# Performance work log

Measured on AMD Instinct MI355X. Metric: run time of the kernel, lower is better.

The kernel has to match this reference:

```python
import jax, jax.numpy as jnp
import numpy as np

B, N, D, H = 4, 4096, 1024, 16
DH = D // H          # per-head dim = 64
M = 256              # number of random features
KEPS = 1e-3          # performer kernel epsilon
LNEPS = 1e-5


def setup_inputs() -> dict:
    key = jax.random.key(0)
    ks = jax.random.split(key, 16)
    s = 0.02
    return {
        "src": jax.random.normal(ks[0], (B, N, D), jnp.float32),
        "Wq": s * jax.random.normal(ks[1], (D, D), jnp.float32),
        "Wk": s * jax.random.normal(ks[2], (D, D), jnp.float32),
        "Wv": s * jax.random.normal(ks[3], (D, D), jnp.float32),
        "Wout": s * jax.random.normal(ks[4], (D, D), jnp.float32),
        "b_out": jnp.zeros((D,), jnp.float32),
        "proj": jax.random.normal(ks[5], (M, DH), jnp.float32),
        "g1": jnp.ones((D,), jnp.float32),
        "beta1": jnp.zeros((D,), jnp.float32),
        "W1": s * jax.random.normal(ks[6], (2048, D), jnp.float32),
        "b1": jnp.zeros((2048,), jnp.float32),
        "W2": s * jax.random.normal(ks[7], (D, 2048), jnp.float32),
        "b2": jnp.zeros((D,), jnp.float32),
        "g2": jnp.ones((D,), jnp.float32),
        "beta2": jnp.zeros((D,), jnp.float32),
    }


def _layernorm(x, g, b):
    mu = x.mean(-1, keepdims=True)
    var = ((x - mu) ** 2).mean(-1, keepdims=True)
    return (x - mu) * jax.lax.rsqrt(var + LNEPS) * g + b


def _softmax_kernel(x, proj, is_query):
    # FAVOR+ positive softmax kernel feature map (performer_pytorch)
    dn = DH ** -0.25           # data normalizer d^{-1/4}
    ratio = M ** -0.5
    data_dash = jnp.einsum('bhnd,md->bhnm', x * dn, proj)
    diag = (x ** 2).sum(-1) * 0.5 * dn * dn            # [b,h,n]
    if is_query:
        stab = data_dash.max(-1, keepdims=True)
    else:
        stab = data_dash.max()
    return ratio * (jnp.exp(data_dash - diag[..., None] - stab) + KEPS)


def reference(src, Wq, Wk, Wv, Wout, b_out, proj, g1, beta1, W1, b1, W2, b2, g2, beta2):
    # ---- Performer self-attention (FAVOR+, non-causal) ----
    def split_heads(x):
        return x.reshape(B, N, H, DH).transpose(0, 2, 1, 3)  # [b,h,n,dh]

    q = split_heads(src @ Wq.T)
    k = split_heads(src @ Wk.T)
    v = split_heads(src @ Wv.T)

    qp = _softmax_kernel(q, proj, is_query=True)   # [b,h,n,m]
    kp = _softmax_kernel(k, proj, is_query=False)  # [b,h,n,m]

    k_sum = kp.sum(-2)                                        # [b,h,m]
    d_inv = 1.0 / jnp.einsum('bhnm,bhm->bhn', qp, k_sum)      # [b,h,n]
    context = jnp.einsum('bhnm,bhnd->bhmd', kp, v)            # [b,h,m,dh]
    attn = jnp.einsum('bhnm,bhmd->bhnd', qp, context) * d_inv[..., None]

    attn = attn.transpose(0, 2, 1, 3).reshape(B, N, D)
    src2 = attn @ Wout.T + b_out

    # ---- residual + norm + FFN (dropout = identity at eval) ----
    x = _layernorm(src + src2, g1, beta1)
    ff = (jax.nn.gelu(x @ W1.T + b1, approximate=False)) @ W2.T + b2
    return _layernorm(x + ff, g2, beta2)
```

## Files before the change

kernel.cpp:

```cpp
#include <hip/hip_runtime.h>

#define DEVI __device__ __forceinline__

using u16 = unsigned short;
using u32 = unsigned int;
using u64 = unsigned long long;

typedef __bf16 bf16x8 __attribute__((ext_vector_type(8)));
typedef float  f32x4  __attribute__((ext_vector_type(4)));

constexpr int BB = 4, NN = 4096, DD = 1024, HH = 16, DH = 64, MF = 256;
constexpr int RT = BB * NN;
constexpr int QKVS = 3072;
constexpr float DN    = 0.35355339059327373f;
constexpr float RATIO = 0.0625f;
constexpr float DIAGC = 0.0625f;
constexpr float KEPSC = 1e-3f;

DEVI u16 f2bf(float f) {
  u32 u = __float_as_uint(f);
  u32 r = u + 0x7fffu + ((u >> 16) & 1u);
  return (u16)(r >> 16);
}
DEVI float bf2f(u16 u) { return __uint_as_float(((u32)u) << 16); }

typedef void __attribute__((address_space(1)))* gas1;
typedef void __attribute__((address_space(3)))* las3;
DEVI void gload_lds16(const void* g, void* l) {
  __builtin_amdgcn_global_load_lds((gas1)(u64)g, (las3)(u32)(u64)l, 16, 0, 0);
}

DEVI bf16x8 ldswz(const u16* base, int row, int kbyte) {
  int p = (row << 7) + kbyte;
  p ^= (row & 7) << 4;
  return *(const bf16x8*)((const char*)base + p);
}

__global__ void cast_kernel(const float* __restrict__ in, u16* __restrict__ out, int n4) {
  int i = blockIdx.x * 256 + threadIdx.x;
  int stride = gridDim.x * 256;
  for (; i < n4; i += stride) {
    float4 v = ((const float4*)in)[i];
    ushort4 o; o.x = f2bf(v.x); o.y = f2bf(v.y); o.z = f2bf(v.z); o.w = f2bf(v.w);
    ((ushort4*)out)[i] = o;
  }
}

__global__ void cast_proj_kernel(const float* __restrict__ in, u16* __restrict__ out) {
  int i = blockIdx.x * 256 + threadIdx.x;
  float4 v = ((const float4*)in)[i];
  ushort4 o; o.x = f2bf(v.x * DN); o.y = f2bf(v.y * DN); o.z = f2bf(v.z * DN); o.w = f2bf(v.w * DN);
  ((ushort4*)out)[i] = o;
}

template <int EPI>
__global__ __launch_bounds__(256, 2) void gemm_bt(
    const u16* __restrict__ A, const u16* __restrict__ Bm,
    u16* __restrict__ Cb, const float* __restrict__ bias,
    int Ncols, int K)
{
  __shared__ __align__(16) u16 sA[128 * 64];
  __shared__ __align__(16) u16 sB[128 * 64];
  const int tid = threadIdx.x, lane = tid & 63;
  const int wv = tid >> 6, wr = wv >> 1, wc = wv & 1;
  const int bm = blockIdx.y, bn = blockIdx.x;

  f32x4 acc[4][4] = {};

  int rowS[4], colS[4], ldsb[4];
#pragma unroll
  for (int it = 0; it < 4; ++it) {
    int p = (it * 256 + tid) * 16;
    ldsb[it] = (it * 256 + (tid & ~63)) * 16;
    int sp = p ^ (((p >> 7) & 7) << 4);
    rowS[it] = sp >> 7;
    colS[it] = (sp >> 1) & 63;
  }
  const size_t baseA = (size_t)bm * 128, baseB = (size_t)bn * 128;

  for (int kt = 0; kt < K; kt += 64) {
#pragma unroll
    for (int it = 0; it < 4; ++it)
      gload_lds16(A + (baseA + rowS[it]) * K + kt + colS[it], (char*)sA + ldsb[it]);
#pragma unroll
    for (int it = 0; it < 4; ++it)
      gload_lds16(Bm + (baseB + rowS[it]) * K + kt + colS[it], (char*)sB + ldsb[it]);
    __syncthreads();
#pragma unroll
    for (int kk = 0; kk < 2; ++kk) {
      const int kbyte = kk * 64 + ((lane >> 4) << 4);
      bf16x8 a[4], b[4];
#pragma unroll
      for (int i = 0; i < 4; ++i) a[i] = ldswz(sA, wr * 64 + i * 16 + (lane & 15), kbyte);
#pragma unroll
      for (int i = 0; i < 4; ++i) b[i] = ldswz(sB, wc * 64 + i * 16 + (lane & 15), kbyte);
#pragma unroll
      for (int i = 0; i < 4; ++i)
#pragma unroll
        for (int j = 0; j < 4; ++j)
          acc[i][j] = __builtin_amdgcn_mfma_f32_16x16x32_bf16(a[i], b[j], acc[i][j], 0, 0, 0);
    }
    __syncthreads();
  }

#pragma unroll
  for (int i = 0; i < 4; ++i) {
    const int gr0 = bm * 128 + wr * 64 + i * 16 + ((lane >> 4) << 2);
#pragma unroll
    for (int j = 0; j < 4; ++j) {
      const int gc = bn * 128 + wc * 64 + j * 16 + (lane & 15);
#pragma unroll
      for (int r = 0; r < 4; ++r) {
        const size_t o = (size_t)(gr0 + r) * Ncols + gc;
        const float v = acc[i][j][r];
        if constexpr (EPI == 0) {
          Cb[o] = f2bf(v);
        } else if constexpr (EPI == 2) {
          float t = v + bias[gc];
          Cb[o] = f2bf(0.5f * t * (1.0f + erff(t * 0.70710678118654752f)));
        } else {
          Cb[o] = f2bf(v + bias[gc]);
        }
      }
    }
  }
}

__global__ __launch_bounds__(256) void kmax_kernel(
    const u16* __restrict__ qkvb, const u16* __restrict__ projb, float* __restrict__ pmax)
{
  __shared__ __align__(16) u16 sX[64 * 72];
  __shared__ float sred[4];
  const int tid = threadIdx.x, lane = tid & 63, wv = tid >> 6;
  const int bh = blockIdx.x, b = bh >> 4, h = bh & 15;
  const int n0 = blockIdx.y * 64;

  for (int i = tid; i < 512; i += 256) {
    int r = i >> 3, c8 = (i & 7) << 3;
    uint4 v = *(const uint4*)(qkvb + ((size_t)(b * NN + n0 + r)) * QKVS + 1024 + h * DH + c8);
    *(uint4*)&sX[r * 72 + c8] = v;
  }
  __syncthreads();

  f32x4 dacc[16] = {};
#pragma unroll
  for (int kk = 0; kk < 2; ++kk) {
    const int ko = kk * 32 + ((lane >> 4) << 3);
    bf16x8 a = *(const bf16x8*)&sX[(wv * 16 + (lane & 15)) * 72 + ko];
#pragma unroll
    for (int f = 0; f < 16; ++f) {
      bf16x8 bb = *(const bf16x8*)(projb + (f * 16 + (lane & 15)) * 64 + ko);
      dacc[f] = __builtin_amdgcn_mfma_f32_16x16x32_bf16(a, bb, dacc[f], 0, 0, 0);
    }
  }
  float mx = -1e30f;
#pragma unroll
  for (int f = 0; f < 16; ++f)
#pragma unroll
    for (int r = 0; r < 4; ++r) mx = fmaxf(mx, dacc[f][r]);
#pragma unroll
  for (int m = 1; m < 64; m <<= 1) mx = fmaxf(mx, __shfl_xor(mx, m));
  if (lane == 0) sred[wv] = mx;
  __syncthreads();
  if (tid == 0)
    pmax[blockIdx.y * gridDim.x + blockIdx.x] =
        fmaxf(fmaxf(sred[0], sred[1]), fmaxf(sred[2], sred[3]));
}

__global__ __launch_bounds__(256) void reduce_max_kernel(
    const float* __restrict__ pmax, float* __restrict__ stab)
{
  const int tid = threadIdx.x;
  float mx = -1e30f;
#pragma unroll
  for (int i = 0; i < 16; ++i) mx = fmaxf(mx, pmax[i * 256 + tid]);
#pragma unroll
  for (int m = 1; m < 64; m <<= 1) mx = fmaxf(mx, __shfl_xor(mx, m));
  __shared__ float sred[4];
  if ((tid & 63) == 0) sred[tid >> 6] = mx;
  __syncthreads();
  if (tid == 0)
    stab[0] = fmaxf(fmaxf(sred[0], sred[1]), fmaxf(sred[2], sred[3]));
}

__global__ __launch_bounds__(256, 1) void kctx_kernel(
    const u16* __restrict__ qkvb, const u16* __restrict__ projb,
    const float* __restrict__ stab_p,
    float* __restrict__ ctxP, float* __restrict__ ksumP2)
{
  __shared__ __align__(16) u16 sX[64 * 72];
  __shared__ __align__(16) u16 sVT[64 * 72];
  __shared__ __align__(16) u16 sKpT[256 * 72];
  __shared__ float sDiag[64];
  const int tid = threadIdx.x, lane = tid & 63, wv = tid >> 6;
  const int bh = blockIdx.x, b = bh >> 4, h = bh & 15;
  const int sl = blockIdx.y;
  const float stab = stab_p[0];

  f32x4 cacc[16] = {};
  float ksacc[16] = {};
  const int row_base = wv * 16 + ((lane >> 4) << 2);

  for (int t = 0; t < 8; ++t) {
    const int n0 = sl * 512 + t * 64;
    if (t) __syncthreads();
    for (int i = tid; i < 512; i += 256) {
      int r = i >> 3, c8 = (i & 7) << 3;
      size_t g = ((size_t)(b * NN + n0 + r)) * QKVS + h * DH + c8;
      uint4 xv = *(const uint4*)(qkvb + g + 1024);
      *(uint4*)&sX[r * 72 + c8] = xv;
      uint4 vv = *(const uint4*)(qkvb + g + 2048);
      const u16* pv = (const u16*)&vv;
#pragma unroll
      for (int j = 0; j < 8; ++j) sVT[(c8 + j) * 72 + r] = pv[j];
    }
    __syncthreads();
    {
      int r = tid >> 2, qq = tid & 3;
      float s = 0;
#pragma unroll
      for (int j = 0; j < 16; ++j) { float x = bf2f(sX[r * 72 + qq * 16 + j]); s += x * x; }
      s += __shfl_xor(s, 1); s += __shfl_xor(s, 2);
      if (qq == 0) sDiag[r] = DIAGC * s;
    }
    f32x4 dacc[16] = {};
#pragma unroll
    for (int kk = 0; kk < 2; ++kk) {
      const int ko = kk * 32 + ((lane >> 4) << 3);
      bf16x8 a = *(const bf16x8*)&sX[(wv * 16 + (lane & 15)) * 72 + ko];
#pragma unroll
      for (int f = 0; f < 16; ++f) {
        bf16x8 bb = *(const bf16x8*)(projb + (f * 16 + (lane & 15)) * 64 + ko);
        dacc[f] = __builtin_amdgcn_mfma_f32_16x16x32_bf16(a, bb, dacc[f], 0, 0, 0);
      }
    }
    __syncthreads();
#pragma unroll
    for (int f = 0; f < 16; ++f) {
      float kvv[4]; float cs = 0;
#pragma unroll
      for (int r = 0; r < 4; ++r) {
        float val = RATIO * (__expf(dacc[f][r] - sDiag[row_base + r] - stab) + KEPSC);
        kvv[r] = val; cs += val;
      }
      cs += __shfl_xor(cs, 16); cs += __shfl_xor(cs, 32);
      ksacc[f] += cs;
      ushort4 pk; pk.x = f2bf(kvv[0]); pk.y = f2bf(kvv[1]); pk.z = f2bf(kvv[2]); pk.w = f2bf(kvv[3]);
      *(ushort4*)&sKpT[(f * 16 + (lane & 15)) * 72 + row_base] = pk;
    }
    __syncthreads();
#pragma unroll
    for (int kk = 0; kk < 2; ++kk) {
      const int ko = kk * 32 + ((lane >> 4) << 3);
      bf16x8 a = *(const bf16x8*)&sVT[(wv * 16 + (lane & 15)) * 72 + ko];
#pragma unroll
      for (int f = 0; f < 16; ++f) {
        bf16x8 bb = *(const bf16x8*)&sKpT[(f * 16 + (lane & 15)) * 72 + ko];
        cacc[f] = __builtin_amdgcn_mfma_f32_16x16x32_bf16(a, bb, cacc[f], 0, 0, 0);
      }
    }
  }
  float* cp = ctxP + (size_t)(sl * 64 + bh) * 16384;
#pragma unroll
  for (int f = 0; f < 16; ++f) {
    const int m = f * 16 + (lane & 15);
#pragma unroll
    for (int r = 0; r < 4; ++r)
      cp[(row_base + r) * 256 + m] = cacc[f][r];
  }
  if (lane < 16) {
    float* kp = ksumP2 + (size_t)((sl * 64 + bh) * 4 + wv) * 256;
#pragma unroll
    for (int f = 0; f < 16; ++f) kp[f * 16 + lane] = ksacc[f];
  }
}

__global__ __launch_bounds__(256) void ctxfin_kernel(
    const float* __restrict__ ctxP, const float* __restrict__ ksumP2,
    u16* __restrict__ ctxb, float* __restrict__ ksum)
{
  const int bid = blockIdx.x, tid = threadIdx.x;
  if (bid < 1024) {
    const int idx = bid * 256 + tid;
    const int bh = idx >> 12, pos = idx & 4095;
    float4 s = {0, 0, 0, 0};
#pragma unroll
    for (int sl = 0; sl < 8; ++sl) {
      float4 v = *(const float4*)(ctxP + (size_t)(sl * 64 + bh) * 16384 + pos * 4);
      s.x += v.x; s.y += v.y; s.z += v.z; s.w += v.w;
    }
    ushort4 o; o.x = f2bf(s.x); o.y = f2bf(s.y); o.z = f2bf(s.z); o.w = f2bf(s.w);
    *(ushort4*)(ctxb + (size_t)bh * 16384 + pos * 4) = o;
  } else {
    const int idx = (bid - 1024) * 256 + tid;
    const int bh = idx >> 8, m = idx & 255;
    float s = 0;
#pragma unroll
    for (int sl = 0; sl < 8; ++sl)
#pragma unroll
      for (int w = 0; w < 4; ++w)
        s += ksumP2[(size_t)((sl * 64 + bh) * 4 + w) * 256 + m];
    ksum[idx] = s;
  }
}

__global__ __launch_bounds__(256, 2) void qattn_kernel(
    const u16* __restrict__ qkvb, const u16* __restrict__ projb,
    const u16* __restrict__ ctxb, const float* __restrict__ ksum,
    u16* __restrict__ attnb)
{
  __shared__ __align__(16) u16 sCtx[64 * 256];
  __shared__ __align__(16) u16 sX[64 * 72];
  __shared__ __align__(16) u16 sQp[64 * 264];
  __shared__ float sKsum[256];
  __shared__ float sDiag[64];
  __shared__ float sDinv[64];
  const int tid = threadIdx.x, lane = tid & 63, wv = tid >> 6;
  const int bh = blockIdx.x, b = bh >> 4, h = bh & 15;

  {
    const char* cbase = (const char*)(ctxb + (size_t)bh * 16384);
#pragma unroll
    for (int it = 0; it < 8; ++it) {
      int p = (it * 256 + tid) * 16;
      int ldsb = (it * 256 + (tid & ~63)) * 16;
      int q = p ^ (((p >> 9) & 7) << 4);
      gload_lds16(cbase + q, (char*)sCtx + ldsb);
    }
  }
  sKsum[tid] = ksum[bh * 256 + tid];

  const int row_base = wv * 16 + ((lane >> 4) << 2);
  const int wr = wv >> 1, wc = wv & 1;

  for (int rt = 0; rt < 2; ++rt) {
    const int n0 = (blockIdx.y * 2 + rt) * 64;
    for (int i = tid; i < 512; i += 256) {
      int r = i >> 3, c8 = (i & 7) << 3;
      uint4 v = *(const uint4*)(qkvb + ((size_t)(b * NN + n0 + r)) * QKVS + h * DH + c8);
      *(uint4*)&sX[r * 72 + c8] = v;
    }
    __syncthreads();
    {
      int r = tid >> 2, qq = tid & 3;
      float s = 0;
#pragma unroll
      for (int j = 0; j < 16; ++j) { float x = bf2f(sX[r * 72 + qq * 16 + j]); s += x * x; }
      s += __shfl_xor(s, 1); s += __shfl_xor(s, 2);
      if (qq == 0) sDiag[r] = DIAGC * s;
    }
    f32x4 dacc[16] = {};
#pragma unroll
    for (int kk = 0; kk < 2; ++kk) {
      const int ko = kk * 32 + ((lane >> 4) << 3);
      bf16x8 a = *(const bf16x8*)&sX[(wv * 16 + (lane & 15)) * 72 + ko];
#pragma unroll
      for (int f = 0; f < 16; ++f) {
        bf16x8 bb = *(const bf16x8*)(projb + (f * 16 + (lane & 15)) * 64 + ko);
        dacc[f] = __builtin_amdgcn_mfma_f32_16x16x32_bf16(a, bb, dacc[f], 0, 0, 0);
      }
    }
    __syncthreads();
#pragma unroll
    for (int r = 0; r < 4; ++r) {
      const int row = row_base + r;
      float mx = dacc[0][r];
#pragma unroll
      for (int f = 1; f < 16; ++f) mx = fmaxf(mx, dacc[f][r]);
      mx = fmaxf(mx, __shfl_xor(mx, 1));
      mx = fmaxf(mx, __shfl_xor(mx, 2));
      mx = fmaxf(mx, __shfl_xor(mx, 4));
      mx = fmaxf(mx, __shfl_xor(mx, 8));
      const float dg = sDiag[row];
      float ds = 0;
#pragma unroll
      for (int f = 0; f < 16; ++f) {
        float qv = RATIO * (__expf(dacc[f][r] - dg - mx) + KEPSC);
        dacc[f][r] = qv;
        ds += qv * sKsum[f * 16 + (lane & 15)];
      }
      ds += __shfl_xor(ds, 1); ds += __shfl_xor(ds, 2);
      ds += __shfl_xor(ds, 4); ds += __shfl_xor(ds, 8);
      if ((lane & 15) == 0) sDinv[row] = 1.0f / ds;
    }
#pragma unroll
    for (int f = 0; f < 16; ++f)
#pragma unroll
      for (int r = 0; r < 4; ++r)
        sQp[(row_base + r) * 264 + f * 16 + (lane & 15)] = f2bf(dacc[f][r]);
    __syncthreads();

    f32x4 acc2[2][2] = {};
#pragma unroll
    for (int kk = 0; kk < 8; ++kk) {
      const int koe = kk * 32 + ((lane >> 4) << 3);
      const int kob = koe * 2;
      bf16x8 a0 = *(const bf16x8*)&sQp[(wr * 32 + (lane & 15)) * 264 + koe];
      bf16x8 a1 = *(const bf16x8*)&sQp[(wr * 32 + 16 + (lane & 15)) * 264 + koe];
      const int j0 = wc * 32 + (lane & 15), j1 = j0 + 16;
      bf16x8 b0 = *(const bf16x8*)((const char*)sCtx + (((j0 << 9) + kob) ^ ((j0 & 7) << 4)));
      bf16x8 b1 = *(const bf16x8*)((const char*)sCtx + (((j1 << 9) + kob) ^ ((j1 & 7) << 4)));
      acc2[0][0] = __builtin_amdgcn_mfma_f32_16x16x32_bf16(a0, b0, acc2[0][0], 0, 0, 0);
      acc2[0][1] = __builtin_amdgcn_mfma_f32_16x16x32_bf16(a0, b1, acc2[0][1], 0, 0, 0);
      acc2[1][0] = __builtin_amdgcn_mfma_f32_16x16x32_bf16(a1, b0, acc2[1][0], 0, 0, 0);
      acc2[1][1] = __builtin_amdgcn_mfma_f32_16x16x32_bf16(a1, b1, acc2[1][1], 0, 0, 0);
    }
#pragma unroll
    for (int mi = 0; mi < 2; ++mi)
#pragma unroll
      for (int ni = 0; ni < 2; ++ni)
#pragma unroll
        for (int r = 0; r < 4; ++r) {
          const int row = wr * 32 + mi * 16 + ((lane >> 4) << 2) + r;
          const int col = wc * 32 + ni * 16 + (lane & 15);
          float v = acc2[mi][ni][r] * sDinv[row];
          attnb[((size_t)(b * NN + n0 + row)) * DD + h * DH + col] = f2bf(v);
        }
    __syncthreads();
  }
}

__global__ __launch_bounds__(256) void ln1_kernel(
    const float* __restrict__ src, const u16* __restrict__ wout,
    const float* __restrict__ g, const float* __restrict__ be, u16* __restrict__ xb)
{
  const int row = blockIdx.x, tid = threadIdx.x;
  const float4 sv = ((const float4*)(src + (size_t)row * DD))[tid];
  const ushort4 wv = ((const ushort4*)(wout + (size_t)row * DD))[tid];
  float x0 = sv.x + bf2f(wv.x);
  float x1 = sv.y + bf2f(wv.y);
  float x2 = sv.z + bf2f(wv.z);
  float x3 = sv.w + bf2f(wv.w);
  float s = x0 + x1 + x2 + x3;
  float ss = x0 * x0 + x1 * x1 + x2 * x2 + x3 * x3;
#pragma unroll
  for (int m = 1; m < 64; m <<= 1) { s += __shfl_xor(s, m); ss += __shfl_xor(ss, m); }
  __shared__ float red[8];
  if ((tid & 63) == 0) { red[tid >> 6] = s; red[4 + (tid >> 6)] = ss; }
  __syncthreads();
  s = red[0] + red[1] + red[2] + red[3];
  ss = red[4] + red[5] + red[6] + red[7];
  const float mu = s * (1.0f / DD);
  const float rs = rsqrtf(ss * (1.0f / DD) - mu * mu + 1e-5f);
  const float4 gv = ((const float4*)g)[tid];
  const float4 bv = ((const float4*)be)[tid];
  ushort4 o;
  o.x = f2bf((x0 - mu) * rs * gv.x + bv.x);
  o.y = f2bf((x1 - mu) * rs * gv.y + bv.y);
  o.z = f2bf((x2 - mu) * rs * gv.z + bv.z);
  o.w = f2bf((x3 - mu) * rs * gv.w + bv.w);
  ((ushort4*)(xb + (size_t)row * DD))[tid] = o;
}

__global__ __launch_bounds__(256) void ln2_kernel(
    const u16* __restrict__ xb, const u16* __restrict__ ff,
    const float* __restrict__ g, const float* __restrict__ be, float* __restrict__ out)
{
  const int row = blockIdx.x, tid = threadIdx.x;
  const ushort4 xv = ((const ushort4*)(xb + (size_t)row * DD))[tid];
  const ushort4 fv = ((const ushort4*)(ff + (size_t)row * DD))[tid];
  float x0 = bf2f(xv.x) + bf2f(fv.x);
  float x1 = bf2f(xv.y) + bf2f(fv.y);
  float x2 = bf2f(xv.z) + bf2f(fv.z);
  float x3 = bf2f(xv.w) + bf2f(fv.w);
  float s = x0 + x1 + x2 + x3;
  float ss = x0 * x0 + x1 * x1 + x2 * x2 + x3 * x3;
#pragma unroll
  for (int m = 1; m < 64; m <<= 1) { s += __shfl_xor(s, m); ss += __shfl_xor(ss, m); }
  __shared__ float red[8];
  if ((tid & 63) == 0) { red[tid >> 6] = s; red[4 + (tid >> 6)] = ss; }
  __syncthreads();
  s = red[0] + red[1] + red[2] + red[3];
  ss = red[4] + red[5] + red[6] + red[7];
  const float mu = s * (1.0f / DD);
  const float rs = rsqrtf(ss * (1.0f / DD) - mu * mu + 1e-5f);
  const float4 gv = ((const float4*)g)[tid];
  const float4 bv = ((const float4*)be)[tid];
  float4 o;
  o.x = (x0 - mu) * rs * gv.x + bv.x;
  o.y = (x1 - mu) * rs * gv.y + bv.y;
  o.z = (x2 - mu) * rs * gv.z + bv.z;
  o.w = (x3 - mu) * rs * gv.w + bv.w;
  ((float4*)(out + (size_t)row * DD))[tid] = o;
}

extern "C" void kernel_launch(void* const* d_in, const int* in_sizes, int n_in,
                              void* d_out, int out_size, void* d_ws, size_t ws_size,
                              hipStream_t stream) {
  (void)in_sizes; (void)n_in; (void)out_size; (void)ws_size;
  const float* src   = (const float*)d_in[0];
  const float* Wq    = (const float*)d_in[1];
  const float* Wk    = (const float*)d_in[2];
  const float* Wv    = (const float*)d_in[3];
  const float* Wout  = (const float*)d_in[4];
  const float* b_out = (const float*)d_in[5];
  const float* proj  = (const float*)d_in[6];
  const float* g1    = (const float*)d_in[7];
  const float* be1   = (const float*)d_in[8];
  const float* W1    = (const float*)d_in[9];
  const float* b1    = (const float*)d_in[10];
  const float* W2    = (const float*)d_in[11];
  const float* b2    = (const float*)d_in[12];
  const float* g2    = (const float*)d_in[13];
  const float* be2   = (const float*)d_in[14];

  char* ws = (char*)d_ws;
  constexpr size_t OFF_SRCB = 0;
  constexpr size_t OFF_QKV  = 33554432;
  constexpr size_t OFF_WOUTB= 100663296;
  constexpr size_t OFF_WQ   = 134217728;
  constexpr size_t OFF_WO   = 140509184;
  constexpr size_t OFF_W1   = 142606336;
  constexpr size_t OFF_W2   = 146800640;
  constexpr size_t OFF_PROJ = 150994944;
  constexpr size_t OFF_CTXB = 151027712;
  constexpr size_t OFF_KSUM = 153124864;
  constexpr size_t OFF_KSP2 = 153190400;
  constexpr size_t OFF_PMAX = 155287552;
  constexpr size_t OFF_STAB = 155303936;

  u16* srcb  = (u16*)(ws + OFF_SRCB);
  u16* qkvb  = (u16*)(ws + OFF_QKV);
  u16* wqkvb = (u16*)(ws + OFF_WQ);
  u16* wob   = (u16*)(ws + OFF_WO);
  u16* w1b   = (u16*)(ws + OFF_W1);
  u16* w2b   = (u16*)(ws + OFF_W2);
  u16* projb = (u16*)(ws + OFF_PROJ);
  u16* ctxb  = (u16*)(ws + OFF_CTXB);
  float* ksum  = (float*)(ws + OFF_KSUM);
  float* ksumP2= (float*)(ws + OFF_KSP2);
  float* pmax  = (float*)(ws + OFF_PMAX);
  float* stab  = (float*)(ws + OFF_STAB);
  float* ctxP  = (float*)(ws + OFF_SRCB);
  u16* attnb = (u16*)(ws + OFF_SRCB);
  u16* woutb = (u16*)(ws + OFF_WOUTB);
  u16* xb    = (u16*)(ws + OFF_QKV + 33554432);
  u16* h1    = (u16*)(ws + OFF_SRCB);
  u16* ff    = (u16*)(ws + OFF_WOUTB);

  cast_kernel<<<4096, 256, 0, stream>>>(src, srcb, RT * DD / 4);
  cast_kernel<<<1024, 256, 0, stream>>>(Wq, wqkvb, DD * DD / 4);
  cast_kernel<<<1024, 256, 0, stream>>>(Wk, wqkvb + DD * DD, DD * DD / 4);
  cast_kernel<<<1024, 256, 0, stream>>>(Wv, wqkvb + 2 * DD * DD, DD * DD / 4);
  cast_kernel<<<1024, 256, 0, stream>>>(Wout, wob, DD * DD / 4);
  cast_kernel<<<2048, 256, 0, stream>>>(W1, w1b, 2048 * DD / 4);
  cast_kernel<<<2048, 256, 0, stream>>>(W2, w2b, 2048 * DD / 4);
  cast_proj_kernel<<<16, 256, 0, stream>>>(proj, projb);

  gemm_bt<0><<<dim3(QKVS / 128, RT / 128), 256, 0, stream>>>(srcb, wqkvb, qkvb, nullptr, QKVS, DD);

  kmax_kernel<<<dim3(64, 64), 256, 0, stream>>>(qkvb, projb, pmax);
  reduce_max_kernel<<<1, 256, 0, stream>>>(pmax, stab);
  kctx_kernel<<<dim3(64, 8), 256, 0, stream>>>(qkvb, projb, stab, ctxP, ksumP2);
  ctxfin_kernel<<<1088, 256, 0, stream>>>(ctxP, ksumP2, ctxb, ksum);
  qattn_kernel<<<dim3(64, 32), 256, 0, stream>>>(qkvb, projb, ctxb, ksum, attnb);

  gemm_bt<3><<<dim3(DD / 128, RT / 128), 256, 0, stream>>>(attnb, wob, woutb, b_out, DD, DD);
  ln1_kernel<<<RT, 256, 0, stream>>>(src, woutb, g1, be1, xb);

  gemm_bt<2><<<dim3(2048 / 128, RT / 128), 256, 0, stream>>>(xb, w1b, h1, b1, 2048, DD);
  gemm_bt<3><<<dim3(DD / 128, RT / 128), 256, 0, stream>>>(h1, w2b, ff, b2, DD, 2048);
  ln2_kernel<<<RT, 256, 0, stream>>>(xb, ff, g2, be2, (float*)d_out);
}
```

Before: 787.0 us.

## Enlarge GEMM tiles, fuse weight casts, atomically reduce context, reuse QKV buffer

The GEMM now uses 512-thread blocks with 256x128 tiles, an lda parameter, and a workgroup swizzle so neighbouring blocks share L2. The six weight casts and the proj cast are merged into one grid-stride kernel. kctx now accumulates the context and k_sum straight into zeroed buffers with atomicAdd, which shrinks ctxfin to a plain bf16 cast. qattn writes its output in place into the Q columns of the QKV buffer, and the output projection reads it with stride 3072. The aim is to cut launch count, partial-sum traffic and A-operand reloads, at the cost of atomic contention, higher register and LDS pressure per block, and nondeterministic float summation.

```diff
diff --git a/kernel.cpp b/kernel.cpp
--- a/kernel.cpp
+++ b/kernel.cpp
@@ -46,44 +46,68 @@
   }
 }
 
-__global__ void cast_proj_kernel(const float* __restrict__ in, u16* __restrict__ out) {
+__global__ void cast_weights_kernel(
+    const float* __restrict__ Wq, const float* __restrict__ Wk,
+    const float* __restrict__ Wv, const float* __restrict__ Wout,
+    const float* __restrict__ W1, const float* __restrict__ W2,
+    const float* __restrict__ proj,
+    u16* __restrict__ wqkvb, u16* __restrict__ wob,
+    u16* __restrict__ w1b, u16* __restrict__ w2b, u16* __restrict__ projb)
+{
+  constexpr int TOT = 2101248;
   int i = blockIdx.x * 256 + threadIdx.x;
-  float4 v = ((const float4*)in)[i];
-  ushort4 o; o.x = f2bf(v.x * DN); o.y = f2bf(v.y * DN); o.z = f2bf(v.z * DN); o.w = f2bf(v.w * DN);
-  ((ushort4*)out)[i] = o;
+  const int stride = gridDim.x * 256;
+  for (; i < TOT; i += stride) {
+    const float* s; u16* d; int loc; float sc = 1.0f;
+    if (i < 1048576) {
+      int seg = i >> 18; loc = i & 262143;
+      s = (seg == 0) ? Wq : (seg == 1) ? Wk : (seg == 2) ? Wv : Wout;
+      d = (seg < 3) ? (wqkvb + seg * 1048576) : wob;
+    } else if (i < 1572864) { loc = i - 1048576; s = W1; d = w1b; }
+    else if (i < 2097152)   { loc = i - 1572864; s = W2; d = w2b; }
+    else                    { loc = i - 2097152; s = proj; d = projb; sc = DN; }
+    float4 v = ((const float4*)s)[loc];
+    ushort4 o; o.x = f2bf(v.x * sc); o.y = f2bf(v.y * sc); o.z = f2bf(v.z * sc); o.w = f2bf(v.w * sc);
+    ((ushort4*)d)[loc] = o;
+  }
 }
 
 template <int EPI>
-__global__ __launch_bounds__(256, 2) void gemm_bt(
-    const u16* __restrict__ A, const u16* __restrict__ Bm,
+__global__ __launch_bounds__(512, 4) void gemm_bt(
+    const u16* __restrict__ A, int lda, const u16* __restrict__ Bm,
     u16* __restrict__ Cb, const float* __restrict__ bias,
     int Ncols, int K)
 {
-  __shared__ __align__(16) u16 sA[128 * 64];
+  __shared__ __align__(16) u16 sA[256 * 64];
   __shared__ __align__(16) u16 sB[128 * 64];
   const int tid = threadIdx.x, lane = tid & 63;
   const int wv = tid >> 6, wr = wv >> 1, wc = wv & 1;
-  const int bm = blockIdx.y, bn = blockIdx.x;
+
+  const int gx = gridDim.x;
+  const int wg = blockIdx.y * gx + blockIdx.x;
+  const int cpx = (gx * gridDim.y) >> 3;
+  const int swz = (wg & 7) * cpx + (wg >> 3);
+  const int bn = swz % gx, bm = swz / gx;
 
   f32x4 acc[4][4] = {};
 
   int rowS[4], colS[4], ldsb[4];
 #pragma unroll
   for (int it = 0; it < 4; ++it) {
-    int p = (it * 256 + tid) * 16;
-    ldsb[it] = (it * 256 + (tid & ~63)) * 16;
+    int p = (it * 512 + tid) * 16;
+    ldsb[it] = (it * 512 + (tid & ~63)) * 16;
     int sp = p ^ (((p >> 7) & 7) << 4);
     rowS[it] = sp >> 7;
     colS[it] = (sp >> 1) & 63;
   }
-  const size_t baseA = (size_t)bm * 128, baseB = (size_t)bn * 128;
+  const size_t baseA = (size_t)bm * 256, baseB = (size_t)bn * 128;
 
   for (int kt = 0; kt < K; kt += 64) {
 #pragma unroll
     for (int it = 0; it < 4; ++it)
-      gload_lds16(A + (baseA + rowS[it]) * K + kt + colS[it], (char*)sA + ldsb[it]);
-#pragma unroll
-    for (int it = 0; it < 4; ++it)
+      gload_lds16(A + (baseA + rowS[it]) * lda + kt + colS[it], (char*)sA + ldsb[it]);
+#pragma unroll
+    for (int it = 0; it < 2; ++it)
       gload_lds16(Bm + (baseB + rowS[it]) * K + kt + colS[it], (char*)sB + ldsb[it]);
     __syncthreads();
 #pragma unroll
@@ -105,7 +129,7 @@
 
 #pragma unroll
   for (int i = 0; i < 4; ++i) {
-    const int gr0 = bm * 128 + wr * 64 + i * 16 + ((lane >> 4) << 2);
+    const int gr0 = bm * 256 + wr * 64 + i * 16 + ((lane >> 4) << 2);
 #pragma unroll
     for (int j = 0; j < 4; ++j) {
       const int gc = bn * 128 + wc * 64 + j * 16 + (lane & 15);
@@ -186,7 +210,7 @@
 __global__ __launch_bounds__(256, 1) void kctx_kernel(
     const u16* __restrict__ qkvb, const u16* __restrict__ projb,
     const float* __restrict__ stab_p,
-    float* __restrict__ ctxP, float* __restrict__ ksumP2)
+    float* __restrict__ ctxT, float* __restrict__ ksum)
 {
   __shared__ __align__(16) u16 sX[64 * 72];
   __shared__ __align__(16) u16 sVT[64 * 72];
@@ -260,54 +284,31 @@
       }
     }
   }
-  float* cp = ctxP + (size_t)(sl * 64 + bh) * 16384;
 #pragma unroll
   for (int f = 0; f < 16; ++f) {
     const int m = f * 16 + (lane & 15);
 #pragma unroll
     for (int r = 0; r < 4; ++r)
-      cp[(row_base + r) * 256 + m] = cacc[f][r];
+      atomicAdd(&ctxT[((size_t)bh * 64 + row_base + r) * 256 + m], cacc[f][r]);
   }
   if (lane < 16) {
-    float* kp = ksumP2 + (size_t)((sl * 64 + bh) * 4 + wv) * 256;
-#pragma unroll
-    for (int f = 0; f < 16; ++f) kp[f * 16 + lane] = ksacc[f];
+#pragma unroll
+    for (int f = 0; f < 16; ++f) atomicAdd(&ksum[bh * 256 + f * 16 + lane], ksacc[f]);
   }
 }
 
 __global__ __launch_bounds__(256) void ctxfin_kernel(
-    const float* __restrict__ ctxP, const float* __restrict__ ksumP2,
-    u16* __restrict__ ctxb, float* __restrict__ ksum)
-{
-  const int bid = blockIdx.x, tid = threadIdx.x;
-  if (bid < 1024) {
-    const int idx = bid * 256 + tid;
-    const int bh = idx >> 12, pos = idx & 4095;
-    float4 s = {0, 0, 0, 0};
-#pragma unroll
-    for (int sl = 0; sl < 8; ++sl) {
-      float4 v = *(const float4*)(ctxP + (size_t)(sl * 64 + bh) * 16384 + pos * 4);
-      s.x += v.x; s.y += v.y; s.z += v.z; s.w += v.w;
-    }
-    ushort4 o; o.x = f2bf(s.x); o.y = f2bf(s.y); o.z = f2bf(s.z); o.w = f2bf(s.w);
-    *(ushort4*)(ctxb + (size_t)bh * 16384 + pos * 4) = o;
-  } else {
-    const int idx = (bid - 1024) * 256 + tid;
-    const int bh = idx >> 8, m = idx & 255;
-    float s = 0;
-#pragma unroll
-    for (int sl = 0; sl < 8; ++sl)
-#pragma unroll
-      for (int w = 0; w < 4; ++w)
-        s += ksumP2[(size_t)((sl * 64 + bh) * 4 + w) * 256 + m];
-    ksum[idx] = s;
-  }
+    const float* __restrict__ ctxT, u16* __restrict__ ctxb)
+{
+  const int i = blockIdx.x * 256 + threadIdx.x;
+  float4 v = ((const float4*)ctxT)[i];
+  ushort4 o; o.x = f2bf(v.x); o.y = f2bf(v.y); o.z = f2bf(v.z); o.w = f2bf(v.w);
+  ((ushort4*)ctxb)[i] = o;
 }
 
 __global__ __launch_bounds__(256, 2) void qattn_kernel(
-    const u16* __restrict__ qkvb, const u16* __restrict__ projb,
-    const u16* __restrict__ ctxb, const float* __restrict__ ksum,
-    u16* __restrict__ attnb)
+    u16* qkvb, const u16* __restrict__ projb,
+    const u16* __restrict__ ctxb, const float* __restrict__ ksum)
 {
   __shared__ __align__(16) u16 sCtx[64 * 256];
   __shared__ __align__(16) u16 sX[64 * 72];
@@ -414,7 +415,7 @@
           const int row = wr * 32 + mi * 16 + ((lane >> 4) << 2) + r;
           const int col = wc * 32 + ni * 16 + (lane & 15);
           float v = acc2[mi][ni][r] * sDinv[row];
-          attnb[((size_t)(b * NN + n0 + row)) * DD + h * DH + col] = f2bf(v);
+          qkvb[((size_t)(b * NN + n0 + row)) * QKVS + h * DH + col] = f2bf(v);
         }
     __syncthreads();
   }
@@ -507,58 +508,52 @@
   char* ws = (char*)d_ws;
   constexpr size_t OFF_SRCB = 0;
   constexpr size_t OFF_QKV  = 33554432;
+  constexpr size_t OFF_XB   = 67108864;
   constexpr size_t OFF_WOUTB= 100663296;
-  constexpr size_t OFF_WQ   = 134217728;
+  constexpr size_t OFF_WQKV = 134217728;
   constexpr size_t OFF_WO   = 140509184;
   constexpr size_t OFF_W1   = 142606336;
   constexpr size_t OFF_W2   = 146800640;
   constexpr size_t OFF_PROJ = 150994944;
-  constexpr size_t OFF_CTXB = 151027712;
-  constexpr size_t OFF_KSUM = 153124864;
-  constexpr size_t OFF_KSP2 = 153190400;
+  constexpr size_t OFF_CTXT = 151027712;
+  constexpr size_t OFF_KSUM = 155222016;
   constexpr size_t OFF_PMAX = 155287552;
   constexpr size_t OFF_STAB = 155303936;
 
   u16* srcb  = (u16*)(ws + OFF_SRCB);
   u16* qkvb  = (u16*)(ws + OFF_QKV);
-  u16* wqkvb = (u16*)(ws + OFF_WQ);
+  u16* wqkvb = (u16*)(ws + OFF_WQKV);
   u16* wob   = (u16*)(ws + OFF_WO);
   u16* w1b   = (u16*)(ws + OFF_W1);
   u16* w2b   = (u16*)(ws + OFF_W2);
   u16* projb = (u16*)(ws + OFF_PROJ);
-  u16* ctxb  = (u16*)(ws + OFF_CTXB);
-  float* ksum  = (float*)(ws + OFF_KSUM);
-  float* ksumP2= (float*)(ws + OFF_KSP2);
-  float* pmax  = (float*)(ws + OFF_PMAX);
-  float* stab  = (float*)(ws + OFF_STAB);
-  float* ctxP  = (float*)(ws + OFF_SRCB);
-  u16* attnb = (u16*)(ws + OFF_SRCB);
+  float* ctxT = (float*)(ws + OFF_CTXT);
+  float* ksum = (float*)(ws + OFF_KSUM);
+  float* pmax = (float*)(ws + OFF_PMAX);
+  float* stab = (float*)(ws + OFF_STAB);
+  u16* ctxb  = (u16*)(ws + OFF_SRCB);
   u16* woutb = (u16*)(ws + OFF_WOUTB);
-  u16* xb    = (u16*)(ws + OFF_QKV + 33554432);
+  u16* xb    = (u16*)(ws + OFF_XB);
   u16* h1    = (u16*)(ws + OFF_SRCB);
   u16* ff    = (u16*)(ws + OFF_WOUTB);
 
   cast_kernel<<<4096, 256, 0, stream>>>(src, srcb, RT * DD / 4);
-  cast_kernel<<<1024, 256, 0, stream>>>(Wq, wqkvb, DD * DD / 4);
-  cast_kernel<<<1024, 256, 0, stream>>>(Wk, wqkvb + DD * DD, DD * DD / 4);
-  cast_kernel<<<1024, 256, 0, stream>>>(Wv, wqkvb + 2 * DD * DD, DD * DD / 4);
-  cast_kernel<<<1024, 256, 0, stream>>>(Wout, wob, DD * DD / 4);
-  cast_kernel<<<2048, 256, 0, stream>>>(W1, w1b, 2048 * DD / 4);
-  cast_kernel<<<2048, 256, 0, stream>>>(W2, w2b, 2048 * DD / 4);
-  cast_proj_kernel<<<16, 256, 0, stream>>>(proj, projb);
-
-  gemm_bt<0><<<dim3(QKVS / 128, RT / 128), 256, 0, stream>>>(srcb, wqkvb, qkvb, nullptr, QKVS, DD);
+  cast_weights_kernel<<<2048, 256, 0, stream>>>(Wq, Wk, Wv, Wout, W1, W2, proj,
+                                                wqkvb, wob, w1b, w2b, projb);
+  hipMemsetAsync(ws + OFF_CTXT, 0, 4194304 + 65536, stream);
+
+  gemm_bt<0><<<dim3(QKVS / 128, RT / 256), 512, 0, stream>>>(srcb, DD, wqkvb, qkvb, nullptr, QKVS, DD);
 
   kmax_kernel<<<dim3(64, 64), 256, 0, stream>>>(qkvb, projb, pmax);
   reduce_max_kernel<<<1, 256, 0, stream>>>(pmax, stab);
-  kctx_kernel<<<dim3(64, 8), 256, 0, stream>>>(qkvb, projb, stab, ctxP, ksumP2);
-  ctxfin_kernel<<<1088, 256, 0, stream>>>(ctxP, ksumP2, ctxb, ksum);
-  qattn_kernel<<<dim3(64, 32), 256, 0, stream>>>(qkvb, projb, ctxb, ksum, attnb);
-
-  gemm_bt<3><<<dim3(DD / 128, RT / 128), 256, 0, stream>>>(attnb, wob, woutb, b_out, DD, DD);
+  kctx_kernel<<<dim3(64, 8), 256, 0, stream>>>(qkvb, projb, stab, ctxT, ksum);
+  ctxfin_kernel<<<4096, 256, 0, stream>>>(ctxT, ctxb);
+  qattn_kernel<<<dim3(64, 32), 256, 0, stream>>>(qkvb, projb, ctxb, ksum);
+
+  gemm_bt<3><<<dim3(DD / 128, RT / 256), 512, 0, stream>>>(qkvb, QKVS, wob, woutb, b_out, DD, DD);
   ln1_kernel<<<RT, 256, 0, stream>>>(src, woutb, g1, be1, xb);
 
-  gemm_bt<2><<<dim3(2048 / 128, RT / 128), 256, 0, stream>>>(xb, w1b, h1, b1, 2048, DD);
-  gemm_bt<3><<<dim3(DD / 128, RT / 128), 256, 0, stream>>>(h1, w2b, ff, b2, DD, 2048);
+  gemm_bt<2><<<dim3(2048 / 128, RT / 256), 512, 0, stream>>>(xb, DD, w1b, h1, b1, 2048, DD);
+  gemm_bt<3><<<dim3(DD / 128, RT / 256), 512, 0, stream>>>(h1, 2048, w2b, ff, b2, DD, 2048);
   ln2_kernel<<<RT, 256, 0, stream>>>(xb, ff, g2, be2, (float*)d_out);
 }
```

Result: faster. 721.3 us (-8.4%).
